# Kernel optimization log

Hardware: AMD Instinct MI355X
Metric: run time of the kernel (lower is better)

## Reference

```python
import jax, jax.numpy as jnp
import numpy as np

B, T, D = 4, 2048, 384
MIN_DUR = 8.0
W_SCALE = 0.02  # keeps softplus output < 8 so clamped+rounded durations are exactly 8


def setup_inputs() -> dict:
    key = jax.random.key(0)
    k_x, k_w1, k_w2 = jax.random.split(key, 3)
    x = jax.random.normal(k_x, (B, T, D), dtype=jnp.float32)
    w1 = jax.random.normal(k_w1, (D, D // 2), dtype=jnp.float32) * W_SCALE
    b1 = jnp.zeros((D // 2,), dtype=jnp.float32)
    w2 = jax.random.normal(k_w2, (D // 2, 1), dtype=jnp.float32) * W_SCALE
    b2 = jnp.zeros((1,), dtype=jnp.float32)
    total_length = B * T * int(MIN_DUR)  # == duration_pred.sum() by construction (all durs clamp to 8)
    return {"x": x, "w1": w1, "b1": b1, "w2": w2, "b2": b2, "total_length": total_length}


def reference(x, w1, b1, w2, b2, total_length):
    # 2-layer MLP duration predictor: Linear -> ReLU -> Linear -> Softplus, squeeze(-1)
    h = jax.nn.relu(jnp.einsum("btd,dh->bth", x, w1) + b1)
    duration_pred = jax.nn.softplus(jnp.einsum("bth,ho->bto", h, w2) + b2)[..., 0]  # (B, T)
    # inference path: clamp to min duration then round
    duration_pred = jnp.round(jnp.maximum(duration_pred, MIN_DUR))
    # Original expands using batch-0 durations for all rows (faithful to source).
    dur0 = duration_pred[0].astype(jnp.int32)            # (T,)
    cum = jnp.cumsum(dur0)                               # (T,) end offsets
    pos = jnp.arange(total_length)                       # static output length
    idx = jnp.minimum(jnp.searchsorted(cum, pos, side="right"), x.shape[1] - 1)
    valid = pos < cum[-1]
    # parallel gather replacing the per-timestep slice-assign loop; zeros past total fill
    expanded = jnp.where(valid[None, :, None], x[:, idx, :], jnp.zeros((), x.dtype))
    return expanded, duration_pred
```

## Files before the change

### kernel.cpp

```cpp
#include <hip/hip_runtime.h>
#include <hip/hip_bf16.h>
#include <math.h>

#define BB 4
#define TT 2048
#define DD 384
#define HH 192
#define TOTAL_LEN 65536
#define EXP_ELEMS (BB * TOTAL_LEN * DD)
#define F4_PER_ROW (DD / 4)
#define TOTAL_F4 (BB * TOTAL_LEN * F4_PER_ROW)
#define ROWS_PER_BLK 16

typedef float f32x4 __attribute__((ext_vector_type(4)));

__global__ __launch_bounds__(256) void mlp_dur_kernel(
    const float* __restrict__ x, const float* __restrict__ w1,
    const float* __restrict__ b1, const float* __restrict__ w2,
    const float* __restrict__ b2, float* __restrict__ dur_out,
    int* __restrict__ dur0) {
  __shared__ float xs[ROWS_PER_BLK * DD];
  __shared__ float part[ROWS_PER_BLK * 4];

  const int tid = threadIdx.x;
  const int lane = tid & 63;
  const int wave = tid >> 6;
  const int row0 = blockIdx.x * ROWS_PER_BLK;

  const f32x4* xg = (const f32x4*)(x + (size_t)row0 * DD);
  f32x4* xs4 = (f32x4*)xs;
#pragma unroll
  for (int i = 0; i < 6; ++i) xs4[i * 256 + tid] = xg[i * 256 + tid];
  __syncthreads();

  float acc[ROWS_PER_BLK];
#pragma unroll
  for (int r = 0; r < ROWS_PER_BLK; ++r) acc[r] = 0.f;

  const int j = tid;
  if (j < HH) {
    for (int k = 0; k < DD; k += 4) {
      float w[4];
#pragma unroll
      for (int kk = 0; kk < 4; ++kk) w[kk] = w1[(size_t)(k + kk) * HH + j];
#pragma unroll
      for (int r = 0; r < ROWS_PER_BLK; ++r) {
        const float* xr = xs + r * DD + k;
#pragma unroll
        for (int kk = 0; kk < 4; ++kk) acc[r] = fmaf(xr[kk], w[kk], acc[r]);
      }
    }
  }

  const float b1v = (j < HH) ? b1[j] : 0.f;
  const float w2v = (j < HH) ? w2[j] : 0.f;

#pragma unroll
  for (int r = 0; r < ROWS_PER_BLK; ++r) {
    float s = fmaxf(acc[r] + b1v, 0.f) * w2v;
#pragma unroll
    for (int off = 32; off > 0; off >>= 1) s += __shfl_down(s, off, 64);
    if (lane == 0) part[r * 4 + wave] = s;
  }
  __syncthreads();

  if (tid < ROWS_PER_BLK) {
    const float z = part[tid * 4] + part[tid * 4 + 1] + part[tid * 4 + 2] +
                    part[tid * 4 + 3] + b2[0];
    const float sp = fmaxf(z, 0.f) + log1pf(expf(-fabsf(z)));
    const float dur = rintf(fmaxf(sp, 8.0f));
    const int row = row0 + tid;
    dur_out[row] = dur;
    if (row < TT) dur0[row] = (int)dur;
  }
}

__global__ __launch_bounds__(256) void scan_kernel(const int* __restrict__ dur0,
                                                   int* __restrict__ cum) {
  __shared__ int lds[256];
  const int tid = threadIdx.x;
  const int base = tid * 8;
  int v[8];
  int run = 0;
#pragma unroll
  for (int i = 0; i < 8; ++i) {
    run += dur0[base + i];
    v[i] = run;
  }
  lds[tid] = run;
  __syncthreads();
  for (int off = 1; off < 256; off <<= 1) {
    const int t = (tid >= off) ? lds[tid - off] : 0;
    __syncthreads();
    lds[tid] += t;
    __syncthreads();
  }
  const int excl = lds[tid] - run;
#pragma unroll
  for (int i = 0; i < 8; ++i) cum[base + i] = v[i] + excl;
}

__global__ __launch_bounds__(256) void idx_kernel(const int* __restrict__ cum,
                                                  int* __restrict__ idx_map) {
  const int pos = blockIdx.x * 256 + threadIdx.x;
  const int total = cum[TT - 1];
  int lo = 0, hi = TT - 1;
  while (lo < hi) {
    const int mid = (lo + hi) >> 1;
    if (cum[mid] > pos) hi = mid;
    else lo = mid + 1;
  }
  idx_map[pos] = (pos < total) ? lo : -1;
}

__global__ __launch_bounds__(256) void expand_kernel(
    const f32x4* __restrict__ x4, const int* __restrict__ idx_map,
    f32x4* __restrict__ out4) {
  const unsigned t = blockIdx.x * 256u + threadIdx.x;
  const unsigned row = t / 96u;
  const unsigned col = t - row * 96u;
  const unsigned b = row >> 16;
  const unsigned pos = row & 65535u;
  const int id = idx_map[pos];
  f32x4 v = {0.f, 0.f, 0.f, 0.f};
  if (id >= 0) v = x4[((size_t)b * TT + (unsigned)id) * F4_PER_ROW + col];
  __builtin_nontemporal_store(v, out4 + t);
}

extern "C" void kernel_launch(void* const* d_in, const int* in_sizes, int n_in,
                              void* d_out, int out_size, void* d_ws,
                              size_t ws_size, hipStream_t stream) {
  const float* x = (const float*)d_in[0];
  const float* w1 = (const float*)d_in[1];
  const float* b1 = (const float*)d_in[2];
  const float* w2 = (const float*)d_in[3];
  const float* b2 = (const float*)d_in[4];

  float* out = (float*)d_out;
  float* dur_out = out + (size_t)EXP_ELEMS;

  int* ws = (int*)d_ws;
  int* dur0 = ws;
  int* cum = ws + TT;
  int* idx_map = ws + 2 * TT;

  mlp_dur_kernel<<<512, 256, 0, stream>>>(x, w1, b1, w2, b2, dur_out, dur0);
  scan_kernel<<<1, 256, 0, stream>>>(dur0, cum);
  idx_kernel<<<TOTAL_LEN / 256, 256, 0, stream>>>(cum, idx_map);
  expand_kernel<<<TOTAL_F4 / 256, 256, 0, stream>>>((const f32x4*)x, idx_map,
                                                    (f32x4*)out);
}
```

Before: 453.1 us.

## Retile MLP per wave, fuse scan into index kernel, grid-stride expand

The MLP kernel now gives each wave 4 rows, with each lane covering 3 hidden columns. This removes the idle fourth wave and the LDS cross-wave reduction, and the softplus is finalized directly by lane 0. The separate scan kernel is folded into the index kernel, so every block redundantly recomputes the 2048-entry prefix sum in LDS, saving a launch. The expand kernel changes from one float4 per thread over a huge grid to a fixed 2048-block grid-stride loop with 48 iterations, which cuts block scheduling overhead but may reduce memory-level parallelism.

```diff
diff --git a/kernel.cpp b/kernel.cpp
--- a/kernel.cpp
+++ b/kernel.cpp
@@ -20,8 +20,6 @@
     const float* __restrict__ b2, float* __restrict__ dur_out,
     int* __restrict__ dur0) {
   __shared__ float xs[ROWS_PER_BLK * DD];
-  __shared__ float part[ROWS_PER_BLK * 4];
-
   const int tid = threadIdx.x;
   const int lane = tid & 63;
   const int wave = tid >> 6;
@@ -33,77 +31,92 @@
   for (int i = 0; i < 6; ++i) xs4[i * 256 + tid] = xg[i * 256 + tid];
   __syncthreads();
 
-  float acc[ROWS_PER_BLK];
+  float acc[4][3];
 #pragma unroll
-  for (int r = 0; r < ROWS_PER_BLK; ++r) acc[r] = 0.f;
+  for (int r = 0; r < 4; ++r)
+#pragma unroll
+    for (int c = 0; c < 3; ++c) acc[r][c] = 0.f;
 
-  const int j = tid;
-  if (j < HH) {
-    for (int k = 0; k < DD; k += 4) {
-      float w[4];
+  const float* xw = xs + (size_t)wave * 4 * DD;
+
+#pragma unroll 2
+  for (int k = 0; k < DD; k += 4) {
+    float w[4][3];
 #pragma unroll
-      for (int kk = 0; kk < 4; ++kk) w[kk] = w1[(size_t)(k + kk) * HH + j];
+    for (int kk = 0; kk < 4; ++kk)
 #pragma unroll
-      for (int r = 0; r < ROWS_PER_BLK; ++r) {
-        const float* xr = xs + r * DD + k;
+      for (int c = 0; c < 3; ++c)
+        w[kk][c] = w1[(size_t)(k + kk) * HH + lane + 64 * c];
+    f32x4 xv[4];
 #pragma unroll
-        for (int kk = 0; kk < 4; ++kk) acc[r] = fmaf(xr[kk], w[kk], acc[r]);
-      }
-    }
+    for (int r = 0; r < 4; ++r)
+      xv[r] = *(const f32x4*)(xw + r * DD + k);
+#pragma unroll
+    for (int r = 0; r < 4; ++r)
+#pragma unroll
+      for (int kk = 0; kk < 4; ++kk)
+#pragma unroll
+        for (int c = 0; c < 3; ++c)
+          acc[r][c] = fmaf(xv[r][kk], w[kk][c], acc[r][c]);
   }
 
-  const float b1v = (j < HH) ? b1[j] : 0.f;
-  const float w2v = (j < HH) ? w2[j] : 0.f;
-
+  float b1v[3], w2v[3];
 #pragma unroll
-  for (int r = 0; r < ROWS_PER_BLK; ++r) {
-    float s = fmaxf(acc[r] + b1v, 0.f) * w2v;
+  for (int c = 0; c < 3; ++c) {
+    b1v[c] = b1[lane + 64 * c];
+    w2v[c] = w2[lane + 64 * c];
+  }
+#pragma unroll
+  for (int r = 0; r < 4; ++r) {
+    float s = 0.f;
+#pragma unroll
+    for (int c = 0; c < 3; ++c)
+      s += fmaxf(acc[r][c] + b1v[c], 0.f) * w2v[c];
 #pragma unroll
     for (int off = 32; off > 0; off >>= 1) s += __shfl_down(s, off, 64);
-    if (lane == 0) part[r * 4 + wave] = s;
-  }
-  __syncthreads();
-
-  if (tid < ROWS_PER_BLK) {
-    const float z = part[tid * 4] + part[tid * 4 + 1] + part[tid * 4 + 2] +
-                    part[tid * 4 + 3] + b2[0];
-    const float sp = fmaxf(z, 0.f) + log1pf(expf(-fabsf(z)));
-    const float dur = rintf(fmaxf(sp, 8.0f));
-    const int row = row0 + tid;
-    dur_out[row] = dur;
-    if (row < TT) dur0[row] = (int)dur;
+    if (lane == 0) {
+      const float z = s + b2[0];
+      const float sp = fmaxf(z, 0.f) + log1pf(expf(-fabsf(z)));
+      const float dur = rintf(fmaxf(sp, 8.0f));
+      const int row = row0 + wave * 4 + r;
+      dur_out[row] = dur;
+      if (row < TT) dur0[row] = (int)dur;
+    }
   }
 }
 
-__global__ __launch_bounds__(256) void scan_kernel(const int* __restrict__ dur0,
-                                                   int* __restrict__ cum) {
-  __shared__ int lds[256];
+__global__ __launch_bounds__(256) void idx_kernel(const int* __restrict__ dur0,
+                                                  int* __restrict__ idx_map) {
+  __shared__ int cum[TT];
+  __shared__ int wsum[256];
   const int tid = threadIdx.x;
-  const int base = tid * 8;
-  int v[8];
+
+  const int4* d4 = (const int4*)dur0;
+  const int4 a = d4[tid * 2];
+  const int4 b = d4[tid * 2 + 1];
+  int v[8] = {a.x, a.y, a.z, a.w, b.x, b.y, b.z, b.w};
   int run = 0;
 #pragma unroll
   for (int i = 0; i < 8; ++i) {
-    run += dur0[base + i];
+    run += v[i];
     v[i] = run;
   }
-  lds[tid] = run;
+  wsum[tid] = run;
   __syncthreads();
   for (int off = 1; off < 256; off <<= 1) {
-    const int t = (tid >= off) ? lds[tid - off] : 0;
+    const int t = (tid >= off) ? wsum[tid - off] : 0;
     __syncthreads();
-    lds[tid] += t;
+    wsum[tid] += t;
     __syncthreads();
   }
-  const int excl = lds[tid] - run;
+  const int excl = wsum[tid] - run;
+  const int base = tid * 8;
 #pragma unroll
   for (int i = 0; i < 8; ++i) cum[base + i] = v[i] + excl;
-}
+  __syncthreads();
 
-__global__ __launch_bounds__(256) void idx_kernel(const int* __restrict__ cum,
-                                                  int* __restrict__ idx_map) {
-  const int pos = blockIdx.x * 256 + threadIdx.x;
   const int total = cum[TT - 1];
+  const int pos = blockIdx.x * 256 + tid;
   int lo = 0, hi = TT - 1;
   while (lo < hi) {
     const int mid = (lo + hi) >> 1;
@@ -116,15 +129,19 @@
 __global__ __launch_bounds__(256) void expand_kernel(
     const f32x4* __restrict__ x4, const int* __restrict__ idx_map,
     f32x4* __restrict__ out4) {
-  const unsigned t = blockIdx.x * 256u + threadIdx.x;
-  const unsigned row = t / 96u;
-  const unsigned col = t - row * 96u;
-  const unsigned b = row >> 16;
-  const unsigned pos = row & 65535u;
-  const int id = idx_map[pos];
-  f32x4 v = {0.f, 0.f, 0.f, 0.f};
-  if (id >= 0) v = x4[((size_t)b * TT + (unsigned)id) * F4_PER_ROW + col];
-  __builtin_nontemporal_store(v, out4 + t);
+  const unsigned stride = 2048u * 256u;
+  unsigned t = blockIdx.x * 256u + threadIdx.x;
+#pragma unroll 4
+  for (int i = 0; i < 48; ++i, t += stride) {
+    const unsigned row = t / 96u;
+    const unsigned col = t - row * 96u;
+    const unsigned b = row >> 16;
+    const unsigned pos = row & 65535u;
+    const int id = idx_map[pos];
+    f32x4 v = {0.f, 0.f, 0.f, 0.f};
+    if (id >= 0) v = x4[((size_t)b * TT + (unsigned)id) * F4_PER_ROW + col];
+    __builtin_nontemporal_store(v, out4 + t);
+  }
 }
 
 extern "C" void kernel_launch(void* const* d_in, const int* in_sizes, int n_in,
@@ -141,12 +158,10 @@
 
   int* ws = (int*)d_ws;
   int* dur0 = ws;
-  int* cum = ws + TT;
   int* idx_map = ws + 2 * TT;
 
   mlp_dur_kernel<<<512, 256, 0, stream>>>(x, w1, b1, w2, b2, dur_out, dur0);
-  scan_kernel<<<1, 256, 0, stream>>>(dur0, cum);
-  idx_kernel<<<TOTAL_LEN / 256, 256, 0, stream>>>(cum, idx_map);
-  expand_kernel<<<TOTAL_F4 / 256, 256, 0, stream>>>((const f32x4*)x, idx_map,
-                                                    (f32x4*)out);
+  idx_kernel<<<TOTAL_LEN / 256, 256, 0, stream>>>(dur0, idx_map);
+  expand_kernel<<<2048, 256, 0, stream>>>((const f32x4*)x, idx_map,
+                                          (f32x4*)out);
 }
```

After: 463.4 us. 2.3% more time.
